# Performance work log

Measured on AMD Instinct MI355X. Metric: run time of the kernel, lower is better.

The kernel has to match this reference:

```python
import jax, jax.numpy as jnp
import numpy as np

# torch.rrelu in eval mode uses slope = (lower+upper)/2 = (1/8 + 1/3)/2
RRELU_SLOPE = (1.0 / 8.0 + 1.0 / 3.0) / 2.0

N_NODES = 50000
N_EDGES = 800000
EMB_FEATS = 128
IN_FEATS = 128
HIDDEN = 64


def setup_inputs() -> dict:
    key = jax.random.key(0)
    ks = jax.random.split(key, 16)
    z = jax.random.normal(ks[0], (N_NODES, EMB_FEATS), dtype=jnp.float32)
    x = jax.random.normal(ks[1], (N_NODES, IN_FEATS), dtype=jnp.float32)
    edge_index = jax.random.randint(ks[2], (2, N_EDGES), 0, N_NODES, dtype=jnp.int32)

    def glorot(k, shape):
        fan_in, fan_out = shape
        lim = jnp.sqrt(6.0 / (fan_in + fan_out))
        return jax.random.uniform(k, shape, jnp.float32, -lim, lim)

    return {
        "z": z,
        "x": x,
        "edge_index": edge_index,
        "W_e1": glorot(ks[3], (EMB_FEATS, HIDDEN)),
        "b_e1": jnp.zeros((HIDDEN,), jnp.float32),
        "W_e2": glorot(ks[4], (HIDDEN, HIDDEN)),
        "b_e2": jnp.zeros((HIDDEN,), jnp.float32),
        "W_f1": glorot(ks[5], (IN_FEATS, HIDDEN)),
        "b_f1": jnp.zeros((HIDDEN,), jnp.float32),
        "W_f2": glorot(ks[6], (HIDDEN, HIDDEN)),
        "b_f2": jnp.zeros((HIDDEN,), jnp.float32),
        "W_out": glorot(ks[7], (HIDDEN, 1)),
        "b_out": jnp.zeros((1,), jnp.float32),
    }


def gcn_conv(h_in, W, b, src, dst, n_nodes):
    """PyG GCNConv: self-loops + symmetric deg^-1/2 normalization."""
    h = h_in @ W  # [N, out]
    # degree of self-loop-augmented graph: indeg + 1
    indeg = jax.ops.segment_sum(
        jnp.ones(dst.shape[0], h.dtype), dst, num_segments=n_nodes)
    deg = indeg + 1.0
    dinv = jnp.where(deg > 0, 1.0 / jnp.sqrt(deg), 0.0)  # [N]
    norm = dinv[src] * dinv[dst]  # [E]
    # neighbor messages (gather + scatter-add)
    agg = jax.ops.segment_sum(h[src] * norm[:, None], dst, num_segments=n_nodes)
    # self-loop contribution: dinv[i]*dinv[i]*h[i]
    agg = agg + h * (dinv * dinv)[:, None]
    return agg + b


def _rrelu(t):
    return jnp.where(t >= 0, t, t * RRELU_SLOPE)


def reference(z, x, edge_index, W_e1, b_e1, W_e2, b_e2,
              W_f1, b_f1, W_f2, b_f2, W_out, b_out):
    src, dst = edge_index[0], edge_index[1]
    n = z.shape[0]
    ze = _rrelu(gcn_conv(z, W_e1, b_e1, src, dst, n))
    ze = jnp.tanh(gcn_conv(ze, W_e2, b_e2, src, dst, n))
    xf = _rrelu(gcn_conv(x, W_f1, b_f1, src, dst, n))
    xf = jnp.tanh(gcn_conv(xf, W_f2, b_f2, src, dst, n))
    return (ze * xf) @ W_out + b_out  # [N, 1]
```

## Files before the change

kernel.cpp:

```cpp
#include <hip/hip_runtime.h>
#include <hip/hip_fp16.h>
#include <math.h>

#define RRELU_SLOPE 0.22916667f


__global__ __launch_bounds__(256) void k_zero(int* __restrict__ cnt, int N) {
    int i = blockIdx.x * 256 + threadIdx.x;
    if (i < N) cnt[i] = 0;
}

__global__ __launch_bounds__(256) void k_deg(const int* __restrict__ dst, int E,
                                             int* __restrict__ cnt,
                                             int* __restrict__ rank) {
    int e = blockIdx.x * 256 + threadIdx.x;
    if (e < E) rank[e] = atomicAdd(&cnt[dst[e]], 1);
}

__global__ __launch_bounds__(256) void k_scan1(const int* __restrict__ cnt, int N,
                                               int* __restrict__ bsum) {
    int i = blockIdx.x * 256 + threadIdx.x;
    int v = (i < N) ? cnt[i] : 0;
    for (int o = 32; o >= 1; o >>= 1) v += __shfl_xor(v, o, 64);
    __shared__ int ws[4];
    if ((threadIdx.x & 63) == 0) ws[threadIdx.x >> 6] = v;
    __syncthreads();
    if (threadIdx.x == 0) bsum[blockIdx.x] = ws[0] + ws[1] + ws[2] + ws[3];
}

__global__ __launch_bounds__(256) void k_scan2(const int* __restrict__ bsum, int NB,
                                               int* __restrict__ boff,
                                               int* __restrict__ rowp, int N, int E) {
    __shared__ int s[256];
    int t = threadIdx.x;
    int v[4];
    int loc = 0;
    for (int i = 0; i < 4; i++) {
        int idx = t * 4 + i;
        v[i] = (idx < NB) ? bsum[idx] : 0;
        loc += v[i];
    }
    s[t] = loc;
    __syncthreads();
    for (int o = 1; o < 256; o <<= 1) {
        int u = (t >= o) ? s[t - o] : 0;
        __syncthreads();
        s[t] += u;
        __syncthreads();
    }
    int excl = s[t] - loc;
    for (int i = 0; i < 4; i++) {
        int idx = t * 4 + i;
        if (idx < NB) { boff[idx] = excl; excl += v[i]; }
    }
    if (t == 0) rowp[N] = E;
}

__global__ __launch_bounds__(256) void k_scan3(const int* __restrict__ cnt,
                                               const int* __restrict__ boff, int N,
                                               int* __restrict__ rowp,
                                               float* __restrict__ dinv) {
    int i = blockIdx.x * 256 + threadIdx.x;
    int lane = threadIdx.x & 63, wid = threadIdx.x >> 6;
    int v = (i < N) ? cnt[i] : 0;
    int inc = v;
    for (int o = 1; o < 64; o <<= 1) {
        int u = __shfl_up(inc, o, 64);
        if (lane >= o) inc += u;
    }
    __shared__ int wsum[4];
    if (lane == 63) wsum[wid] = inc;
    __syncthreads();
    int wo = 0;
    for (int w = 0; w < wid; w++) wo += wsum[w];
    if (i < N) {
        int excl = inc - v + wo + boff[blockIdx.x];
        rowp[i] = excl;
        dinv[i] = 1.0f / sqrtf((float)v + 1.0f);
    }
}

__global__ __launch_bounds__(256) void k_fill(const int* __restrict__ src,
                                              const int* __restrict__ dst,
                                              const int* __restrict__ rank, int E,
                                              const int* __restrict__ rowp,
                                              int* __restrict__ csrc) {
    int e = blockIdx.x * 256 + threadIdx.x;
    if (e >= E) return;
    int d = dst[e];
    csrc[rowp[d] + rank[e]] = src[e];
}

__global__ __launch_bounds__(256) void k_mm1(const float* __restrict__ A0,
                                             const float* __restrict__ A1,
                                             const float* __restrict__ W0,
                                             const float* __restrict__ W1,
                                             const float* __restrict__ dinv,
                                             __half* __restrict__ Hh, int N) {
    const float* A = blockIdx.y ? A1 : A0;
    const float* W = blockIdx.y ? W1 : W0;
    __half* H = Hh + (size_t)blockIdx.y * N * 64;

    __shared__ float As[64][20];
    __shared__ float Ws[16][64];

    const int tid = threadIdx.x;
    const int tc = tid & 15, tr = tid >> 4;
    const int row0 = blockIdx.x * 64;
    const int srow = tid >> 2, sk = (tid & 3) * 4;
    const int wk = tid >> 4, wc = (tid & 15) * 4;

    float acc[4][4] = {};

    for (int k0 = 0; k0 < 128; k0 += 16) {
        float4 av = make_float4(0.f, 0.f, 0.f, 0.f);
        int gr = row0 + srow;
        if (gr < N) av = *(const float4*)(A + (size_t)gr * 128 + k0 + sk);
        float4 wv = *(const float4*)(W + (size_t)(k0 + wk) * 64 + wc);
        __syncthreads();
        *(float4*)&As[srow][sk] = av;
        *(float4*)&Ws[wk][wc] = wv;
        __syncthreads();

#pragma unroll
        for (int k = 0; k < 16; k += 4) {
            float4 a4[4], w4[4];
#pragma unroll
            for (int i = 0; i < 4; i++) a4[i] = *(const float4*)&As[tr * 4 + i][k];
#pragma unroll
            for (int kk = 0; kk < 4; kk++) w4[kk] = *(const float4*)&Ws[k + kk][tc * 4];
#pragma unroll
            for (int i = 0; i < 4; i++) {
                const float* ap = (const float*)&a4[i];
#pragma unroll
                for (int kk = 0; kk < 4; kk++) {
                    const float* wp = (const float*)&w4[kk];
                    float a = ap[kk];
                    acc[i][0] = fmaf(a, wp[0], acc[i][0]);
                    acc[i][1] = fmaf(a, wp[1], acc[i][1]);
                    acc[i][2] = fmaf(a, wp[2], acc[i][2]);
                    acc[i][3] = fmaf(a, wp[3], acc[i][3]);
                }
            }
        }
    }

#pragma unroll
    for (int i = 0; i < 4; i++) {
        int r = row0 + tr * 4 + i;
        if (r < N) {
            float dv = dinv[r];
            union { __half2 h2[2]; uint2 u; } pk;
            pk.h2[0] = __floats2half2_rn(acc[i][0] * dv, acc[i][1] * dv);
            pk.h2[1] = __floats2half2_rn(acc[i][2] * dv, acc[i][3] * dv);
            *(uint2*)(H + (size_t)r * 64 + tc * 4) = pk.u;
        }
    }
}

__global__ __launch_bounds__(256) void k_mm2h(const __half* __restrict__ A0,
                                              const __half* __restrict__ A1,
                                              const float* __restrict__ W0,
                                              const float* __restrict__ W1,
                                              const float* __restrict__ dinv,
                                              __half* __restrict__ Hh, int N) {
    const __half* A = blockIdx.y ? A1 : A0;
    const float* W = blockIdx.y ? W1 : W0;
    __half* H = Hh + (size_t)blockIdx.y * N * 64;

    __shared__ float As[64][20];
    __shared__ float Ws[16][64];

    const int tid = threadIdx.x;
    const int tc = tid & 15, tr = tid >> 4;
    const int row0 = blockIdx.x * 64;
    const int srow = tid >> 2, sk = (tid & 3) * 4;
    const int wk = tid >> 4, wc = (tid & 15) * 4;

    float acc[4][4] = {};

    for (int k0 = 0; k0 < 64; k0 += 16) {
        float4 av = make_float4(0.f, 0.f, 0.f, 0.f);
        int gr = row0 + srow;
        if (gr < N) {
            union { uint2 u; __half2 h2[2]; } cu;
            cu.u = *(const uint2*)(A + (size_t)gr * 64 + k0 + sk);
            float2 f01 = __half22float2(cu.h2[0]);
            float2 f23 = __half22float2(cu.h2[1]);
            av = make_float4(f01.x, f01.y, f23.x, f23.y);
        }
        float4 wv = *(const float4*)(W + (size_t)(k0 + wk) * 64 + wc);
        __syncthreads();
        *(float4*)&As[srow][sk] = av;
        *(float4*)&Ws[wk][wc] = wv;
        __syncthreads();

#pragma unroll
        for (int k = 0; k < 16; k += 4) {
            float4 a4[4], w4[4];
#pragma unroll
            for (int i = 0; i < 4; i++) a4[i] = *(const float4*)&As[tr * 4 + i][k];
#pragma unroll
            for (int kk = 0; kk < 4; kk++) w4[kk] = *(const float4*)&Ws[k + kk][tc * 4];
#pragma unroll
            for (int i = 0; i < 4; i++) {
                const float* ap = (const float*)&a4[i];
#pragma unroll
                for (int kk = 0; kk < 4; kk++) {
                    const float* wp = (const float*)&w4[kk];
                    float a = ap[kk];
                    acc[i][0] = fmaf(a, wp[0], acc[i][0]);
                    acc[i][1] = fmaf(a, wp[1], acc[i][1]);
                    acc[i][2] = fmaf(a, wp[2], acc[i][2]);
                    acc[i][3] = fmaf(a, wp[3], acc[i][3]);
                }
            }
        }
    }

#pragma unroll
    for (int i = 0; i < 4; i++) {
        int r = row0 + tr * 4 + i;
        if (r < N) {
            float dv = dinv[r];
            union { __half2 h2[2]; uint2 u; } pk;
            pk.h2[0] = __floats2half2_rn(acc[i][0] * dv, acc[i][1] * dv);
            pk.h2[1] = __floats2half2_rn(acc[i][2] * dv, acc[i][3] * dv);
            *(uint2*)(H + (size_t)r * 64 + tc * 4) = pk.u;
        }
    }
}

#define GATHER_ADD(S, C)                                       \
    {                                                          \
        union { uint2 u; __half2 h2[2]; } g_;                  \
        g_.u = *(const uint2*)(Hp + (size_t)(C) * 64);         \
        float2 a_ = __half22float2(g_.h2[0]);                  \
        float2 b_ = __half22float2(g_.h2[1]);                  \
        S.x += a_.x; S.y += a_.y; S.z += b_.x; S.w += b_.y;    \
    }

#define AGG_LOOP()                                                          \
    int beg = rowp[i], end = rowp[i + 1];                                   \
    float4 s0 = {0.f, 0.f, 0.f, 0.f}, s1 = {0.f, 0.f, 0.f, 0.f};           \
    int p = beg;                                                            \
    if ((p & 1) && p < end) {                                               \
        if (lane < 32) { int c = csrc[p]; GATHER_ADD(s0, c); }              \
        p++;                                                                \
    }                                                                       \
    for (; p + 4 <= end; p += 4) {                                          \
        int2 c01 = *(const int2*)(csrc + p);                                \
        int2 c23 = *(const int2*)(csrc + p + 2);                            \
        int cA = (lane < 32) ? c01.x : c01.y;                               \
        int cB = (lane < 32) ? c23.x : c23.y;                               \
        GATHER_ADD(s0, cA);                                                 \
        GATHER_ADD(s1, cB);                                                 \
    }                                                                       \
    if (p + 2 <= end) {                                                     \
        int2 c01 = *(const int2*)(csrc + p);                                \
        int cA = (lane < 32) ? c01.x : c01.y;                               \
        GATHER_ADD(s0, cA);                                                 \
        p += 2;                                                             \
    }                                                                       \
    if (p < end) {                                                          \
        if (lane < 32) { int c = csrc[p]; GATHER_ADD(s1, c); }              \
    }                                                                       \
    float4 s;                                                               \
    s.x = s0.x + s1.x; s.y = s0.y + s1.y;                                   \
    s.z = s0.z + s1.z; s.w = s0.w + s1.w;                                   \
    s.x += __shfl_xor(s.x, 32, 64);                                         \
    s.y += __shfl_xor(s.y, 32, 64);                                         \
    s.z += __shfl_xor(s.z, 32, 64);                                         \
    s.w += __shfl_xor(s.w, 32, 64);

__global__ __launch_bounds__(256) void k_agg_act(
    const int* __restrict__ rowp, const int* __restrict__ csrc,
    const float* __restrict__ dinv, const __half* __restrict__ Hh, int N,
    const float* __restrict__ bz, const float* __restrict__ bx,
    __half* __restrict__ azh, __half* __restrict__ axh) {
    int wid = threadIdx.x >> 6, lane = threadIdx.x & 63;
    int i = blockIdx.x * 4 + wid;
    if (i >= N) return;
    int f0 = (lane & 15) * 4;
    int plane = (lane >> 4) & 1;
    const __half* Hp = Hh + (size_t)plane * N * 64 + f0;
    AGG_LOOP();

    if (lane < 32) {
        float4 sl = {0.f, 0.f, 0.f, 0.f};
        GATHER_ADD(sl, i);
        float dvi = dinv[i];
        const float* bb = plane ? bx : bz;
        float4 b = *(const float4*)(bb + f0);
        float r0 = fmaf(dvi, s.x + sl.x, b.x);
        float r1 = fmaf(dvi, s.y + sl.y, b.y);
        float r2 = fmaf(dvi, s.z + sl.z, b.z);
        float r3 = fmaf(dvi, s.w + sl.w, b.w);
        r0 = r0 >= 0.f ? r0 : r0 * RRELU_SLOPE;
        r1 = r1 >= 0.f ? r1 : r1 * RRELU_SLOPE;
        r2 = r2 >= 0.f ? r2 : r2 * RRELU_SLOPE;
        r3 = r3 >= 0.f ? r3 : r3 * RRELU_SLOPE;
        __half* ap = plane ? axh : azh;
        union { __half2 h2[2]; uint2 u; } pk;
        pk.h2[0] = __floats2half2_rn(r0, r1);
        pk.h2[1] = __floats2half2_rn(r2, r3);
        *(uint2*)(ap + (size_t)i * 64 + f0) = pk.u;
    }
}

__global__ __launch_bounds__(256) void k_agg_final(
    const int* __restrict__ rowp, const int* __restrict__ csrc,
    const float* __restrict__ dinv, const __half* __restrict__ Hh, int N,
    const float* __restrict__ bz, const float* __restrict__ bx,
    const float* __restrict__ Wout, const float* __restrict__ bout,
    float* __restrict__ out) {
    int wid = threadIdx.x >> 6, lane = threadIdx.x & 63;
    int i = blockIdx.x * 4 + wid;
    if (i >= N) return;
    int f0 = (lane & 15) * 4;
    int plane = (lane >> 4) & 1;
    const __half* Hp = Hh + (size_t)plane * N * 64 + f0;
    AGG_LOOP();

    float4 sl = {0.f, 0.f, 0.f, 0.f};
    if (lane < 32) GATHER_ADD(sl, i);
    float dvi = dinv[i];
    const float* bb = plane ? bx : bz;
    float4 b = *(const float4*)(bb + f0);
    float t0 = tanhf(fmaf(dvi, s.x + sl.x, b.x));
    float t1 = tanhf(fmaf(dvi, s.y + sl.y, b.y));
    float t2 = tanhf(fmaf(dvi, s.z + sl.z, b.z));
    float t3 = tanhf(fmaf(dvi, s.w + sl.w, b.w));
    float q0 = __shfl_xor(t0, 16, 64);
    float q1 = __shfl_xor(t1, 16, 64);
    float q2 = __shfl_xor(t2, 16, 64);
    float q3 = __shfl_xor(t3, 16, 64);
    float4 w = *(const float4*)(Wout + f0);
    float prod = t0 * q0 * w.x + t1 * q1 * w.y + t2 * q2 * w.z + t3 * q3 * w.w;
    for (int o = 8; o >= 1; o >>= 1) prod += __shfl_xor(prod, o, 64);
    if (lane == 0) out[i] = prod + bout[0];
}


extern "C" void kernel_launch(void* const* d_in, const int* in_sizes, int n_in,
                              void* d_out, int out_size, void* d_ws, size_t ws_size,
                              hipStream_t stream) {
    const float* z = (const float*)d_in[0];
    const float* x = (const float*)d_in[1];
    const int* ei = (const int*)d_in[2];
    const float* We1 = (const float*)d_in[3];
    const float* be1 = (const float*)d_in[4];
    const float* We2 = (const float*)d_in[5];
    const float* be2 = (const float*)d_in[6];
    const float* Wf1 = (const float*)d_in[7];
    const float* bf1 = (const float*)d_in[8];
    const float* Wf2 = (const float*)d_in[9];
    const float* bf2 = (const float*)d_in[10];
    const float* Wout = (const float*)d_in[11];
    const float* bout = (const float*)d_in[12];
    float* out = (float*)d_out;

    int N = in_sizes[0] / 128;
    int E = in_sizes[2] / 2;
    const int* src = ei;
    const int* dst = ei + E;

    char* base = (char*)d_ws;
    size_t off = 0;
    auto take = [&](size_t nbytes) -> char* {
        char* p = base + off;
        off = (off + nbytes + 255) & ~(size_t)255;
        return p;
    };
    int NB = (N + 255) / 256;
    int* cnt = (int*)take((size_t)N * 4);
    int* bsum = (int*)take(1024 * 4);
    int* boff = (int*)take(1024 * 4);
    int* rowp = (int*)take(((size_t)N + 1) * 4);
    float* dinv = (float*)take((size_t)N * 4);
    int* rank = (int*)take((size_t)E * 4);
    int* csrc = (int*)take((size_t)E * 4);
    __half* Hh = (__half*)take((size_t)N * 64 * 2 * 2);
    __half* azh = (__half*)take((size_t)N * 64 * 2);
    __half* axh = (__half*)take((size_t)N * 64 * 2);

    int egrid = (E + 255) / 256;
    k_zero<<<NB, 256, 0, stream>>>(cnt, N);
    k_deg<<<egrid, 256, 0, stream>>>(dst, E, cnt, rank);
    k_scan1<<<NB, 256, 0, stream>>>(cnt, N, bsum);
    k_scan2<<<1, 256, 0, stream>>>(bsum, NB, boff, rowp, N, E);
    k_scan3<<<NB, 256, 0, stream>>>(cnt, boff, N, rowp, dinv);
    k_fill<<<egrid, 256, 0, stream>>>(src, dst, rank, E, rowp, csrc);

    dim3 mmgrid((N + 63) / 64, 2);
    int agrid = (N + 3) / 4;

    k_mm1<<<mmgrid, 256, 0, stream>>>(z, x, We1, Wf1, dinv, Hh, N);
    k_agg_act<<<agrid, 256, 0, stream>>>(rowp, csrc, dinv, Hh, N, be1, bf1, azh, axh);
    k_mm2h<<<mmgrid, 256, 0, stream>>>(azh, axh, We2, Wf2, dinv, Hh, N);
    k_agg_final<<<agrid, 256, 0, stream>>>(rowp, csrc, dinv, Hh, N, be2, bf2, Wout,
                                           bout, out);
}
```

Before: 195.3 us.

## Interleave z/x feature planes per node and widen aggregation gathers to 16 bytes

The two half-precision feature matrices now sit interleaved in one buffer with a 128-element row per node, so one node's z and x features are contiguous. The aggregation kernels load 16 bytes (8 halves) per lane, and 16 lanes cover a full node row. The wavefront's four lane groups handle four different edges at once, with four independent accumulators, and the groups are combined with shuffles afterwards. This is meant to cut the number of scattered gather transactions and raise memory-level parallelism per edge. The cost is more registers per lane and some lanes sitting idle on tail edges.

```diff
diff --git a/kernel.cpp b/kernel.cpp
--- a/kernel.cpp
+++ b/kernel.cpp
@@ -99,7 +99,7 @@
                                              __half* __restrict__ Hh, int N) {
     const float* A = blockIdx.y ? A1 : A0;
     const float* W = blockIdx.y ? W1 : W0;
-    __half* H = Hh + (size_t)blockIdx.y * N * 64;
+    __half* H = Hh + blockIdx.y * 64;
 
     __shared__ float As[64][20];
     __shared__ float Ws[16][64];
@@ -153,7 +153,7 @@
             union { __half2 h2[2]; uint2 u; } pk;
             pk.h2[0] = __floats2half2_rn(acc[i][0] * dv, acc[i][1] * dv);
             pk.h2[1] = __floats2half2_rn(acc[i][2] * dv, acc[i][3] * dv);
-            *(uint2*)(H + (size_t)r * 64 + tc * 4) = pk.u;
+            *(uint2*)(H + (size_t)r * 128 + tc * 4) = pk.u;
         }
     }
 }
@@ -166,7 +166,7 @@
                                               __half* __restrict__ Hh, int N) {
     const __half* A = blockIdx.y ? A1 : A0;
     const float* W = blockIdx.y ? W1 : W0;
-    __half* H = Hh + (size_t)blockIdx.y * N * 64;
+    __half* H = Hh + blockIdx.y * 64;
 
     __shared__ float As[64][20];
     __shared__ float Ws[16][64];
@@ -226,52 +226,64 @@
             union { __half2 h2[2]; uint2 u; } pk;
             pk.h2[0] = __floats2half2_rn(acc[i][0] * dv, acc[i][1] * dv);
             pk.h2[1] = __floats2half2_rn(acc[i][2] * dv, acc[i][3] * dv);
-            *(uint2*)(H + (size_t)r * 64 + tc * 4) = pk.u;
+            *(uint2*)(H + (size_t)r * 128 + tc * 4) = pk.u;
         }
     }
 }
 
-#define GATHER_ADD(S, C)                                       \
+#define GATHER_ADD8(S, C)                                      \
     {                                                          \
-        union { uint2 u; __half2 h2[2]; } g_;                  \
-        g_.u = *(const uint2*)(Hp + (size_t)(C) * 64);         \
-        float2 a_ = __half22float2(g_.h2[0]);                  \
-        float2 b_ = __half22float2(g_.h2[1]);                  \
-        S.x += a_.x; S.y += a_.y; S.z += b_.x; S.w += b_.y;    \
+        union { uint4 u; __half2 h2[4]; } g_;                  \
+        g_.u = *(const uint4*)(Hp + (size_t)(C) * 128);        \
+        float2 f0_ = __half22float2(g_.h2[0]);                 \
+        float2 f1_ = __half22float2(g_.h2[1]);                 \
+        float2 f2_ = __half22float2(g_.h2[2]);                 \
+        float2 f3_ = __half22float2(g_.h2[3]);                 \
+        S[0] += f0_.x; S[1] += f0_.y; S[2] += f1_.x;           \
+        S[3] += f1_.y; S[4] += f2_.x; S[5] += f2_.y;           \
+        S[6] += f3_.x; S[7] += f3_.y;                          \
     }
 
 #define AGG_LOOP()                                                          \
     int beg = rowp[i], end = rowp[i + 1];                                   \
-    float4 s0 = {0.f, 0.f, 0.f, 0.f}, s1 = {0.f, 0.f, 0.f, 0.f};           \
+    float s0[8] = {}, s1[8] = {}, s2[8] = {}, s3[8] = {};                   \
     int p = beg;                                                            \
-    if ((p & 1) && p < end) {                                               \
-        if (lane < 32) { int c = csrc[p]; GATHER_ADD(s0, c); }              \
-        p++;                                                                \
+    for (; p + 16 <= end; p += 16) {                                        \
+        int cA = csrc[p + e];                                               \
+        int cB = csrc[p + 4 + e];                                           \
+        int cC = csrc[p + 8 + e];                                           \
+        int cD = csrc[p + 12 + e];                                          \
+        GATHER_ADD8(s0, cA);                                                \
+        GATHER_ADD8(s1, cB);                                                \
+        GATHER_ADD8(s2, cC);                                                \
+        GATHER_ADD8(s3, cD);                                                \
     }                                                                       \
-    for (; p + 4 <= end; p += 4) {                                          \
-        int2 c01 = *(const int2*)(csrc + p);                                \
-        int2 c23 = *(const int2*)(csrc + p + 2);                            \
-        int cA = (lane < 32) ? c01.x : c01.y;                               \
-        int cB = (lane < 32) ? c23.x : c23.y;                               \
-        GATHER_ADD(s0, cA);                                                 \
-        GATHER_ADD(s1, cB);                                                 \
+    for (; p + 8 <= end; p += 8) {                                          \
+        int cA = csrc[p + e];                                               \
+        int cB = csrc[p + 4 + e];                                           \
+        GATHER_ADD8(s0, cA);                                                \
+        GATHER_ADD8(s1, cB);                                                \
     }                                                                       \
-    if (p + 2 <= end) {                                                     \
-        int2 c01 = *(const int2*)(csrc + p);                                \
-        int cA = (lane < 32) ? c01.x : c01.y;                               \
-        GATHER_ADD(s0, cA);                                                 \
-        p += 2;                                                             \
+    if (p + 4 <= end) {                                                     \
+        int cA = csrc[p + e];                                               \
+        GATHER_ADD8(s0, cA);                                                \
+        p += 4;                                                             \
     }                                                                       \
-    if (p < end) {                                                          \
-        if (lane < 32) { int c = csrc[p]; GATHER_ADD(s1, c); }              \
+    {                                                                       \
+        int rem = end - p;                                                  \
+        if (rem > 0) {                                                      \
+            int c = csrc[p + ((e < rem) ? e : 0)];                          \
+            if (e < rem) GATHER_ADD8(s1, c);                                \
+        }                                                                   \
     }                                                                       \
-    float4 s;                                                               \
-    s.x = s0.x + s1.x; s.y = s0.y + s1.y;                                   \
-    s.z = s0.z + s1.z; s.w = s0.w + s1.w;                                   \
-    s.x += __shfl_xor(s.x, 32, 64);                                         \
-    s.y += __shfl_xor(s.y, 32, 64);                                         \
-    s.z += __shfl_xor(s.z, 32, 64);                                         \
-    s.w += __shfl_xor(s.w, 32, 64);
+    float s[8];                                                             \
+    _Pragma("unroll")                                                       \
+    for (int k = 0; k < 8; k++)                                             \
+        s[k] = (s0[k] + s1[k]) + (s2[k] + s3[k]);                           \
+    _Pragma("unroll")                                                       \
+    for (int k = 0; k < 8; k++) s[k] += __shfl_xor(s[k], 16, 64);           \
+    _Pragma("unroll")                                                       \
+    for (int k = 0; k < 8; k++) s[k] += __shfl_xor(s[k], 32, 64);
 
 __global__ __launch_bounds__(256) void k_agg_act(
     const int* __restrict__ rowp, const int* __restrict__ csrc,
@@ -281,30 +293,35 @@
     int wid = threadIdx.x >> 6, lane = threadIdx.x & 63;
     int i = blockIdx.x * 4 + wid;
     if (i >= N) return;
-    int f0 = (lane & 15) * 4;
-    int plane = (lane >> 4) & 1;
-    const __half* Hp = Hh + (size_t)plane * N * 64 + f0;
+    int g = lane & 7;
+    int h = (lane >> 3) & 1;
+    int e = lane >> 4;
+    const __half* Hp = Hh + h * 64 + g * 8;
     AGG_LOOP();
 
-    if (lane < 32) {
-        float4 sl = {0.f, 0.f, 0.f, 0.f};
-        GATHER_ADD(sl, i);
+    if (e == 0) {
+        float sl[8] = {};
+        GATHER_ADD8(sl, i);
         float dvi = dinv[i];
-        const float* bb = plane ? bx : bz;
-        float4 b = *(const float4*)(bb + f0);
-        float r0 = fmaf(dvi, s.x + sl.x, b.x);
-        float r1 = fmaf(dvi, s.y + sl.y, b.y);
-        float r2 = fmaf(dvi, s.z + sl.z, b.z);
-        float r3 = fmaf(dvi, s.w + sl.w, b.w);
-        r0 = r0 >= 0.f ? r0 : r0 * RRELU_SLOPE;
-        r1 = r1 >= 0.f ? r1 : r1 * RRELU_SLOPE;
-        r2 = r2 >= 0.f ? r2 : r2 * RRELU_SLOPE;
-        r3 = r3 >= 0.f ? r3 : r3 * RRELU_SLOPE;
-        __half* ap = plane ? axh : azh;
-        union { __half2 h2[2]; uint2 u; } pk;
-        pk.h2[0] = __floats2half2_rn(r0, r1);
-        pk.h2[1] = __floats2half2_rn(r2, r3);
-        *(uint2*)(ap + (size_t)i * 64 + f0) = pk.u;
+        const float* bb = h ? bx : bz;
+        float4 b0 = *(const float4*)(bb + g * 8);
+        float4 b1 = *(const float4*)(bb + g * 8 + 4);
+        float r[8];
+        const float* bp = (const float*)&b0;
+#pragma unroll
+        for (int k = 0; k < 4; k++) r[k] = fmaf(dvi, s[k] + sl[k], bp[k]);
+        bp = (const float*)&b1;
+#pragma unroll
+        for (int k = 0; k < 4; k++) r[4 + k] = fmaf(dvi, s[4 + k] + sl[4 + k], bp[k]);
+#pragma unroll
+        for (int k = 0; k < 8; k++) r[k] = r[k] >= 0.f ? r[k] : r[k] * RRELU_SLOPE;
+        __half* ap = h ? axh : azh;
+        union { __half2 h2[4]; uint4 u; } pk;
+        pk.h2[0] = __floats2half2_rn(r[0], r[1]);
+        pk.h2[1] = __floats2half2_rn(r[2], r[3]);
+        pk.h2[2] = __floats2half2_rn(r[4], r[5]);
+        pk.h2[3] = __floats2half2_rn(r[6], r[7]);
+        *(uint4*)(ap + (size_t)i * 64 + g * 8) = pk.u;
     }
 }
 
@@ -317,27 +334,37 @@
     int wid = threadIdx.x >> 6, lane = threadIdx.x & 63;
     int i = blockIdx.x * 4 + wid;
     if (i >= N) return;
-    int f0 = (lane & 15) * 4;
-    int plane = (lane >> 4) & 1;
-    const __half* Hp = Hh + (size_t)plane * N * 64 + f0;
+    int g = lane & 7;
+    int h = (lane >> 3) & 1;
+    int e = lane >> 4;
+    const __half* Hp = Hh + h * 64 + g * 8;
     AGG_LOOP();
 
-    float4 sl = {0.f, 0.f, 0.f, 0.f};
-    if (lane < 32) GATHER_ADD(sl, i);
+    float sl[8] = {};
+    GATHER_ADD8(sl, i);
     float dvi = dinv[i];
-    const float* bb = plane ? bx : bz;
-    float4 b = *(const float4*)(bb + f0);
-    float t0 = tanhf(fmaf(dvi, s.x + sl.x, b.x));
-    float t1 = tanhf(fmaf(dvi, s.y + sl.y, b.y));
-    float t2 = tanhf(fmaf(dvi, s.z + sl.z, b.z));
-    float t3 = tanhf(fmaf(dvi, s.w + sl.w, b.w));
-    float q0 = __shfl_xor(t0, 16, 64);
-    float q1 = __shfl_xor(t1, 16, 64);
-    float q2 = __shfl_xor(t2, 16, 64);
-    float q3 = __shfl_xor(t3, 16, 64);
-    float4 w = *(const float4*)(Wout + f0);
-    float prod = t0 * q0 * w.x + t1 * q1 * w.y + t2 * q2 * w.z + t3 * q3 * w.w;
-    for (int o = 8; o >= 1; o >>= 1) prod += __shfl_xor(prod, o, 64);
+    const float* bb = h ? bx : bz;
+    float4 b0 = *(const float4*)(bb + g * 8);
+    float4 b1 = *(const float4*)(bb + g * 8 + 4);
+    float t[8];
+    const float* bp = (const float*)&b0;
+#pragma unroll
+    for (int k = 0; k < 4; k++) t[k] = tanhf(fmaf(dvi, s[k] + sl[k], bp[k]));
+    bp = (const float*)&b1;
+#pragma unroll
+    for (int k = 0; k < 4; k++)
+        t[4 + k] = tanhf(fmaf(dvi, s[4 + k] + sl[4 + k], bp[k]));
+    float4 w0 = *(const float4*)(Wout + g * 8);
+    float4 w1 = *(const float4*)(Wout + g * 8 + 4);
+    float prod = 0.f;
+    const float* wp = (const float*)&w0;
+#pragma unroll
+    for (int k = 0; k < 4; k++) prod = fmaf(t[k] * __shfl_xor(t[k], 8, 64), wp[k], prod);
+    wp = (const float*)&w1;
+#pragma unroll
+    for (int k = 0; k < 4; k++)
+        prod = fmaf(t[4 + k] * __shfl_xor(t[4 + k], 8, 64), wp[k], prod);
+    for (int o = 4; o >= 1; o >>= 1) prod += __shfl_xor(prod, o, 64);
     if (lane == 0) out[i] = prod + bout[0];
 }
 
@@ -380,7 +407,7 @@
     float* dinv = (float*)take((size_t)N * 4);
     int* rank = (int*)take((size_t)E * 4);
     int* csrc = (int*)take((size_t)E * 4);
-    __half* Hh = (__half*)take((size_t)N * 64 * 2 * 2);
+    __half* Hh = (__half*)take((size_t)N * 128 * 2);
     __half* azh = (__half*)take((size_t)N * 64 * 2);
     __half* axh = (__half*)take((size_t)N * 64 * 2);
 
```

Result: faster. 187.4 us (median of 3 runs) (-4.0%).
